# Kernel optimization log

Measured on AMD Instinct MI355X. Metric: run time of the kernel, lower is better.

## Reference

```python
import jax, jax.numpy as jnp
import numpy as np

IMG = 128                  # img_size
FMM = 35.0
SENSOR = 32.0
FUV = FMM * IMG / SENSOR   # focal length in pixels (screen space, in_ndc=False)
N_PTS = 16384
CHUNK = 1024               # points per scan step
R_SIL = 0.008              # silhouette pass radius (NDC)
R_DEP = 0.012              # depth pass radius (NDC)
K_SIL = 8
K_DEP = 16
DIST = 1.2


def _look_at(dist, elev_deg, azim_deg):
    # PyTorch3D look_at_view_transform with at=origin, up=+Y, degrees=True
    elev = jnp.deg2rad(elev_deg)
    azim = jnp.deg2rad(azim_deg)
    cam = jnp.stack([dist * jnp.cos(elev) * jnp.sin(azim),
                     dist * jnp.sin(elev),
                     dist * jnp.cos(elev) * jnp.cos(azim)], axis=-1)  # (B,3)
    up = jnp.array([0.0, 1.0, 0.0], dtype=cam.dtype)
    z_ax = -cam / (jnp.linalg.norm(cam, axis=-1, keepdims=True) + 1e-8)
    x_ax = jnp.cross(jnp.broadcast_to(up, z_ax.shape), z_ax)
    x_ax = x_ax / (jnp.linalg.norm(x_ax, axis=-1, keepdims=True) + 1e-8)
    y_ax = jnp.cross(z_ax, x_ax)
    R = jnp.stack([x_ax, y_ax, z_ax], axis=-1)   # columns are camera axes
    T = -jnp.einsum('bi,bij->bj', cam, R)        # X_cam = X_world @ R + T
    return R, T


def _project(pts, R, T):
    # world -> camera (row-vector convention) -> screen px -> PyTorch3D NDC
    Xc = jnp.einsum('bni,bij->bnj', pts, R) + T[:, None, :]
    z = Xc[..., 2]
    z_safe = jnp.where(z > 1e-5, z, 1.0)  # points behind camera are culled anyway
    xs = FUV * Xc[..., 0] / z_safe + IMG / 2.0
    ys = FUV * Xc[..., 1] / z_safe + IMG / 2.0
    x_ndc = 1.0 - 2.0 * xs / IMG
    y_ndc = 1.0 - 2.0 * ys / IMG
    return jnp.stack([x_ndc, y_ndc], axis=-1), z


def _rasterize(xy, z, r2, K):
    """Per-pixel K nearest-in-depth points within per-point NDC radius.
    xy: (B,N,2) NDC, z: (B,N) camera depth, r2: (B,N) squared radius.
    Returns zbuf, dists of shape (B,IMG,IMG,K), -1 for empty slots."""
    B, N, _ = xy.shape
    P = IMG * IMG
    # pixel-center NDC grid (PyTorch3D: +X left, +Y up; row-major flatten)
    gxs = 1.0 - (2.0 * jnp.arange(IMG, dtype=xy.dtype) + 1.0) / IMG  # per column
    gys = 1.0 - (2.0 * jnp.arange(IMG, dtype=xy.dtype) + 1.0) / IMG  # per row
    gx = jnp.tile(gxs, IMG)          # (P,)
    gy = jnp.repeat(gys, IMG)        # (P,)

    nch = N // CHUNK
    px = xy[..., 0].reshape(B, nch, CHUNK).swapaxes(0, 1)
    py = xy[..., 1].reshape(B, nch, CHUNK).swapaxes(0, 1)
    pz = z.reshape(B, nch, CHUNK).swapaxes(0, 1)
    pr2 = r2.reshape(B, nch, CHUNK).swapaxes(0, 1)

    def body(carry, c):
        top_z, top_d = carry
        cx, cy, cz, cr2 = c                               # each (B,CHUNK)
        dx = gx[None, :, None] - cx[:, None, :]           # (B,P,CHUNK)
        dy = gy[None, :, None] - cy[:, None, :]
        d2 = dx * dx + dy * dy
        ok = (d2 < cr2[:, None, :]) & (cz[:, None, :] > 0.0)
        zc = jnp.where(ok, cz[:, None, :], jnp.inf)
        cand_z = jnp.concatenate([top_z, zc], axis=-1)    # (B,P,K+CHUNK)
        cand_d = jnp.concatenate([top_d, d2], axis=-1)
        negz, idx = jax.lax.top_k(-cand_z, K)             # K smallest depths
        return (-negz, jnp.take_along_axis(cand_d, idx, axis=-1)), None

    init = (jnp.full((B, P, K), jnp.inf, dtype=xy.dtype),
            jnp.zeros((B, P, K), dtype=xy.dtype))
    (top_z, top_d), _ = jax.lax.scan(jax.checkpoint(body), init, (px, py, pz, pr2))
    valid = jnp.isfinite(top_z)
    zbuf = jnp.where(valid, top_z, -1.0).reshape(B, IMG, IMG, K)
    dists = jnp.where(valid, top_d, -1.0).reshape(B, IMG, IMG, K)
    return zbuf, dists


def setup_inputs() -> dict:
    key = jax.random.key(0)
    k1, k2 = jax.random.split(key)
    point_cloud = jax.random.normal(k1, (2, N_PTS, 6), dtype=jnp.float32) * 0.25
    param = jax.random.normal(k2, (2, 8, 3), dtype=jnp.float32) * 20.0  # degrees
    return {"point_cloud": point_cloud, "param": param}


def reference(point_cloud, param):
    pts = point_cloud[..., :3]
    B = pts.shape[0]
    elev0 = param[:, 1, 0]
    azim0 = param[:, 0, 0]

    # ---- silhouette pass (radius 0.008, K=8) + alpha compositing ----
    R0, T0 = _look_at(DIST, elev0, azim0)
    xy0, z0 = _project(pts, R0, T0)
    r2_sil = jnp.full((B, N_PTS), R_SIL * R_SIL, dtype=pts.dtype)
    _, dists_s = _rasterize(xy0, z0, r2_sil, K_SIL)
    alphas = jnp.where(dists_s >= 0.0, 1.0 - dists_s / (R_SIL * R_SIL), 0.0)
    trans = jnp.cumprod(1.0 - alphas, axis=-1)
    trans_excl = jnp.concatenate([jnp.ones_like(trans[..., :1]), trans[..., :-1]], axis=-1)
    sihlt_map = jnp.sum(alphas * trans_excl, axis=-1, keepdims=True) * 255.0  # (B,H,W,1)

    # ---- depth pass with random view (radius 0.012, K=16) ----
    kd = jax.random.key(42)
    ke, ka = jax.random.split(kd)
    elev_d = jax.random.uniform(ke, (B,), dtype=pts.dtype) * 60.0 - 30.0
    azim_d = jax.random.uniform(ka, (B,), dtype=pts.dtype) * 300.0 + azim0 + 30.0
    Rd, Td = _look_at(DIST, elev_d, azim_d)
    xyd, zd = _project(pts, Rd, Td)
    r2_dep = jnp.full((B, N_PTS), R_DEP * R_DEP, dtype=pts.dtype)
    zbuf_d, _ = _rasterize(xyd, zd, r2_dep, K_DEP)
    depth_ini = zbuf_d[..., 0]

    # density-aware adaptive radius (detached, per source .detach())
    area = jnp.sum((jax.lax.stop_gradient(depth_ini) > 0.0).astype(pts.dtype), axis=(1, 2))
    pa_radius = area / 16384.0 * 0.057                      # (B,)
    r2_ada = jnp.broadcast_to((pa_radius * pa_radius)[:, None], (B, N_PTS))

    zbuf_a, dists_a = _rasterize(xyd, zd, r2_ada, K_DEP)
    depth_img = zbuf_a[..., :8]
    dist_top = dists_a[..., :8]
    return (sihlt_map, depth_img, dist_top)
```

## Files before the change

### kernel.cpp

```cpp
#include <hip/hip_runtime.h>
#include <hip/hip_cooperative_groups.h>
#include <cstring>
#include <cstdint>

namespace cg = cooperative_groups;

#define NPTS 16384
#define FUVC 140.0f
#define R_SILF 0.008f
#define R_DEPF 0.012f
#define R2_SIL (0.008f*0.008f)
#define R2_DEP (0.012f*0.012f)
#define CH 512

#define AREA_OFF  48
#define PA_OFF    50
#define R2ADA_OFF 52
#define TICK0     54
#define TICK1     55
#define CNT_SIL   64
#define OFF_SIL   2112
#define CNT_ADA   4160
#define OFF_ADA   6208
#define FLAGS8    8256
#define FLAGS     8256
#define ZERO_END  16448
#define PROJ0     41024
#define PROJ1     172096
#define LSILF     303168
#define LADAF     827456
#define WS1_WORDS 2007104u
#define WS1_NEEDED ((size_t)WS1_WORDS * 4u)
#define LSIL      303168
#define LADA      434240
#define WS2_WORDS 729152u
#define WS2_NEEDED ((size_t)WS2_WORDS * 4u)

#define FUSED_BLOCKS 1024
#define FUSED_NT (FUSED_BLOCKS * 256)

__device__ __forceinline__ void cam_calc(float elev, float azim, float c[12]) {
    const float D2R = 0.017453292519943295f;
    float er = elev * D2R, ar = azim * D2R;
    float ce = cosf(er), se = sinf(er), ca = cosf(ar), sa = sinf(ar);
    float cx = 1.2f * ce * sa, cy = 1.2f * se, cz = 1.2f * ce * ca;
    float n = sqrtf(cx*cx + cy*cy + cz*cz) + 1e-8f;
    float zx = -cx / n, zy = -cy / n, zz = -cz / n;
    float xx = zz, xy = 0.0f, xz = -zx;
    float xn = sqrtf(xx*xx + xy*xy + xz*xz) + 1e-8f;
    xx /= xn; xz /= xn;
    float yx = zy*xz - zz*xy, yy = zz*xx - zx*xz, yz = zx*xy - zy*xx;
    c[0]=xx; c[1]=xy; c[2]=xz; c[3]=yx; c[4]=yy; c[5]=yz;
    c[6]=zx; c[7]=zy; c[8]=zz;
    c[9]  = -(cx*xx + cy*xy + cz*xz);
    c[10] = -(cx*yx + cy*yy + cz*yz);
    c[11] = -(cx*zx + cy*zy + cz*zz);
}

__device__ __forceinline__ void cam_compute(const float* __restrict__ param,
                                            float* __restrict__ ws,
                                            int t, float ue0, float ue1,
                                            float ua0, float ua1) {
    int b = t >> 1, cam = t & 1;
    float azim0 = param[b * 24 + 0];
    float elev0 = param[b * 24 + 3];
    float elev, azim;
    if (cam == 0) { elev = elev0; azim = azim0; }
    else {
        float ue = b ? ue1 : ue0;
        float ua = b ? ua1 : ua0;
        elev = ue * 60.0f - 30.0f;
        azim = ua * 300.0f + azim0 + 30.0f;
    }
    float c[12];
    cam_calc(elev, azim, c);
    float* w = ws + t * 12;
    #pragma unroll
    for (int i = 0; i < 12; i++) w[i] = c[i];
}

__device__ __forceinline__ float4 project_pt(const float* __restrict__ P,
                                             const float c[12]) {
    float X = P[0], Y = P[1], Z = P[2];
    float xc = X*c[0] + Y*c[1] + Z*c[2] + c[9];
    float yc = X*c[3] + Y*c[4] + Z*c[5] + c[10];
    float zc = X*c[6] + Y*c[7] + Z*c[8] + c[11];
    float zs = zc > 1e-5f ? zc : 1.0f;
    float px = 1.0f - (FUVC * xc / zs + 64.0f) * (1.0f/64.0f);
    float py = 1.0f - (FUVC * yc / zs + 64.0f) * (1.0f/64.0f);
    return make_float4(px, py, zc, 0.0f);
}

__device__ __forceinline__ void pix_range(float p, float r, int& lo, int& hi) {
    float lo_f = (1.0f - p - r) * 64.0f - 0.5f;
    float hi_f = (1.0f - p + r) * 64.0f - 0.5f;
    lo = (int)ceilf(lo_f - 1e-3f);
    hi = (int)floorf(hi_f + 1e-3f);
    lo = max(lo, 0); hi = min(hi, 127);
}

__device__ __forceinline__ void bin_bbox(float4 q, float r, int& bxl, int& bxh,
                                         int& byl, int& byh) {
    bxl = 0; bxh = -1; byl = 0; byh = -1;
    if (q.z > 0.0f) {
        int cl, chh, rl, rh;
        pix_range(q.x, r, cl, chh);
        pix_range(q.y, r, rl, rh);
        if (cl <= chh && rl <= rh) {
            bxl = cl >> 2; bxh = chh >> 2; byl = rl >> 2; byh = rh >> 2;
        }
    }
}

__device__ __forceinline__ void top8_insert(float z, float d,
                                            float tz[8], float td[8]) {
    #pragma unroll
    for (int k = 0; k < 8; k++) {
        bool lt = z < tz[k];
        float oz = tz[k], od = td[k];
        if (lt) { tz[k] = z; td[k] = d; z = oz; d = od; }
    }
}

__device__ __forceinline__ void hit_test(float4 pt, float gx, float gy, float r2,
                                         float tz[8], float td[8]) {
    float dx = gx - pt.x, dy = gy - pt.y;
    float d2 = dx*dx + dy*dy;
    if (d2 < r2 && pt.z > 0.0f && pt.z < tz[7]) top8_insert(pt.z, d2, tz, td);
}

__device__ __forceinline__ void merge_sorted8(float tz[8], float td[8], int mask) {
    float oz[8], od[8];
    #pragma unroll
    for (int k = 0; k < 8; k++) {
        oz[k] = __shfl_xor(tz[k], mask);
        od[k] = __shfl_xor(td[k], mask);
    }
    float mz[8], md[8];
    #pragma unroll
    for (int k = 0; k < 8; k++) {
        bool take = oz[7 - k] < tz[k];
        mz[k] = take ? oz[7 - k] : tz[k];
        md[k] = take ? od[7 - k] : td[k];
    }
    #define CE(i, j) { bool sw = mz[j] < mz[i]; \
        float t1 = mz[i], t2 = md[i]; \
        mz[i] = sw ? mz[j] : mz[i]; md[i] = sw ? md[j] : md[i]; \
        mz[j] = sw ? t1 : mz[j];    md[j] = sw ? t2 : md[j]; }
    CE(0,4) CE(1,5) CE(2,6) CE(3,7)
    CE(0,2) CE(1,3) CE(4,6) CE(5,7)
    CE(0,1) CE(2,3) CE(4,5) CE(6,7)
    #undef CE
    #pragma unroll
    for (int k = 0; k < 8; k++) { tz[k] = mz[k]; td[k] = md[k]; }
}

__device__ __forceinline__ void scan1024(unsigned* uw, unsigned cbase,
                                         unsigned obase, unsigned* s, int t) {
    unsigned c0 = uw[cbase + t*4 + 0];
    unsigned c1 = uw[cbase + t*4 + 1];
    unsigned c2 = uw[cbase + t*4 + 2];
    unsigned c3 = uw[cbase + t*4 + 3];
    unsigned tot = c0 + c1 + c2 + c3;
    s[t] = tot; __syncthreads();
    for (int off = 1; off < 256; off <<= 1) {
        unsigned v = (t >= off) ? s[t - off] : 0u;
        __syncthreads();
        s[t] += v;
        __syncthreads();
    }
    unsigned base = s[t] - tot;
    uw[obase + t*4 + 0] = base;
    uw[obase + t*4 + 1] = base + c0;
    uw[obase + t*4 + 2] = base + c0 + c1;
    uw[obase + t*4 + 3] = base + c0 + c1 + c2;
    uw[cbase + t*4 + 0] = 0;
    uw[cbase + t*4 + 1] = 0;
    uw[cbase + t*4 + 2] = 0;
    uw[cbase + t*4 + 3] = 0;
}

__device__ __forceinline__ void body_area_scan(float* __restrict__ ws, int job,
                                               int t, unsigned* s) {
    unsigned* uw = (unsigned*)ws;
    if (job < 2) {
        int b = job;
        unsigned acc = 0;
        #pragma unroll
        for (int j = 0; j < 16; j++) {
            unsigned w = uw[FLAGS8 + b * 4096 + t * 16 + j];
            acc += __popc(w & 0x01010101u);
        }
        s[t] = acc; __syncthreads();
        for (int off = 128; off > 0; off >>= 1) {
            if (t < off) s[t] += s[t + off];
            __syncthreads();
        }
        if (t == 0) {
            unsigned area = s[0];
            uw[AREA_OFF + b] = area;
            float pa = (float)area * (1.0f/16384.0f) * 0.057f;
            ws[PA_OFF + b] = pa;
            ws[R2ADA_OFF + b] = pa * pa;
        }
    } else {
        int b = job - 2;
        scan1024(uw, CNT_SIL + b * 1024, OFF_SIL + b * 1024, s, t);
    }
}

__device__ __forceinline__ void body_cnt_ada(float* __restrict__ ws, int p) {
    unsigned* uw = (unsigned*)ws;
    int b = p >> 14;
    float4 q = ((const float4*)(ws + PROJ1))[p];
    float pa = ws[PA_OFF + b];
    int bxl, bxh, byl, byh;
    bin_bbox(q, pa, bxl, bxh, byl, byh);
    for (int by = byl; by <= byh; by++)
        for (int bx = bxl; bx <= bxh; bx++)
            atomicAdd(&uw[CNT_ADA + b * 1024 + by * 32 + bx], 1u);
}

__device__ __forceinline__ void body_scat_sil(float* __restrict__ ws, int p) {
    unsigned* uw = (unsigned*)ws;
    int b = p >> 14;
    float4 q = ((const float4*)(ws + PROJ0))[p];
    int bxl, bxh, byl, byh;
    bin_bbox(q, R_SILF, bxl, bxh, byl, byh);
    for (int by = byl; by <= byh; by++)
        for (int bx = bxl; bx <= bxh; bx++) {
            unsigned bin = b * 1024 + by * 32 + bx;
            unsigned idx = uw[OFF_SIL + bin] + atomicAdd(&uw[CNT_SIL + bin], 1u);
            ((float4*)(ws + LSILF))[b * 65536 + idx] = q;
        }
}

__device__ __forceinline__ void body_scan_ada(float* __restrict__ ws, int b, int t) {
    unsigned* uw = (unsigned*)ws;
    unsigned c[16]; unsigned tot = 0;
    #pragma unroll
    for (int j = 0; j < 16; j++) { c[j] = uw[CNT_ADA + b * 1024 + t * 16 + j]; tot += c[j]; }
    unsigned inc = tot;
    #pragma unroll
    for (int off = 1; off < 64; off <<= 1) {
        unsigned v = __shfl_up(inc, off);
        if (t >= off) inc += v;
    }
    unsigned base = inc - tot;
    #pragma unroll
    for (int j = 0; j < 16; j++) {
        uw[OFF_ADA + b * 1024 + t * 16 + j] = base;
        base += c[j];
        uw[CNT_ADA + b * 1024 + t * 16 + j] = 0u;
    }
}

__device__ __forceinline__ void body_scat_ada(float* __restrict__ ws, int p) {
    unsigned* uw = (unsigned*)ws;
    int b = p >> 14;
    float4 q = ((const float4*)(ws + PROJ1))[p];
    float pa = ws[PA_OFF + b];
    int bxl, bxh, byl, byh;
    bin_bbox(q, pa, bxl, bxh, byl, byh);
    for (int by = byl; by <= byh; by++)
        for (int bx = bxl; bx <= bxh; bx++) {
            unsigned bin = b * 1024 + by * 32 + bx;
            unsigned idx = uw[OFF_ADA + bin] + atomicAdd(&uw[CNT_ADA + bin], 1u);
            ((float4*)(ws + LADAF))[b * 147456 + idx] = q;
        }
}

__device__ __forceinline__ void body_gather(const float* __restrict__ ws,
                                            float* __restrict__ out,
                                            int id, int lane) {
    const unsigned* uw = (const unsigned*)ws;
    bool sil = id < 2048;
    int gt = sil ? id : id - 2048;
    int b = gt >> 10;
    int tile = gt & 1023;
    int p = lane & 15, s = lane >> 4;
    int bx = tile & 31, by = tile >> 5;
    int col = (bx << 2) + (p & 3), row = (by << 2) + (p >> 2);
    float gx = 1.0f - (float)(2*col + 1) * (1.0f/128.0f);
    float gy = 1.0f - (float)(2*row + 1) * (1.0f/128.0f);
    float r2 = sil ? R2_SIL : ws[R2ADA_OFF + b];
    unsigned start = sil ? uw[OFF_SIL + b * 1024 + tile] : uw[OFF_ADA + b * 1024 + tile];
    unsigned len   = sil ? uw[CNT_SIL + b * 1024 + tile] : uw[CNT_ADA + b * 1024 + tile];
    const float4* lst = sil ? ((const float4*)(ws + LSILF)) + b * 65536 + start
                            : ((const float4*)(ws + LADAF)) + b * 147456 + start;

    float tz[8], td[8];
    #pragma unroll
    for (int k = 0; k < 8; k++) { tz[k] = INFINITY; td[k] = 0.0f; }

    unsigned i = (unsigned)s;
    while (i + 28 < len) {
        float4 cb[8];
        #pragma unroll
        for (int u = 0; u < 8; u++) cb[u] = lst[i + 4u * (unsigned)u];
        #pragma unroll
        for (int u = 0; u < 8; u++) hit_test(cb[u], gx, gy, r2, tz, td);
        i += 32;
    }
    for (; i < len; i += 4) hit_test(lst[i], gx, gy, r2, tz, td);

    merge_sorted8(tz, td, 16);
    merge_sorted8(tz, td, 32);

    if (s == 0) {
        int pix = (b << 14) + row * 128 + col;
        if (sil) {
            float trans = 1.0f, acc = 0.0f;
            #pragma unroll
            for (int k = 0; k < 8; k++) {
                float a = (tz[k] != INFINITY) ? (1.0f - td[k] / R2_SIL) : 0.0f;
                acc += a * trans;
                trans *= (1.0f - a);
            }
            out[pix] = acc * 255.0f;
        } else {
            float* dep = out + 32768  + (size_t)pix * 8;
            float* dst = out + 294912 + (size_t)pix * 8;
            #pragma unroll
            for (int k = 0; k < 8; k++) {
                bool v = (tz[k] != INFINITY);
                dep[k] = v ? tz[k] : -1.0f;
                dst[k] = v ? td[k] : -1.0f;
            }
        }
    }
}

__global__ __launch_bounds__(256) void k_fusedp(const float* __restrict__ pc,
                                                const float* __restrict__ param,
                                                float* __restrict__ ws,
                                                float* __restrict__ out,
                                                float ue0, float ue1,
                                                float ua0, float ua1) {
    cg::grid_group grid = cg::this_grid();
    unsigned* uw = (unsigned*)ws;
    __shared__ unsigned sh[2048];
    __shared__ unsigned shLast;
    int t = threadIdx.x;
    int tid = blockIdx.x * 256 + t;

    for (int i = 48 + tid; i < ZERO_END; i += FUSED_NT) uw[i] = 0u;
    if (tid < 4) cam_compute(param, ws, tid, ue0, ue1, ua0, ua1);
    grid.sync();

    if (blockIdx.x < 128) {
        int b = blockIdx.x >> 6;
        int p = ((blockIdx.x & 63) << 8) + t;
        unsigned char* fb = (unsigned char*)(uw + FLAGS8);
        const float* P = pc + ((size_t)b * NPTS + p) * 6;
        float c0[12], c1[12];
        const float* w0 = ws + (b * 2) * 12;
        #pragma unroll
        for (int i = 0; i < 12; i++) { c0[i] = w0[i]; c1[i] = w0[12 + i]; }

        #pragma unroll
        for (int j = 0; j < 4; j++) sh[t * 4 + j] = 0u;
        __syncthreads();

        float4 q0 = project_pt(P, c0);
        ((float4*)(ws + PROJ0))[b * NPTS + p] = q0;
        int bxl, bxh, byl, byh;
        bin_bbox(q0, R_SILF, bxl, bxh, byl, byh);
        for (int by = byl; by <= byh; by++)
            for (int bx = bxl; bx <= bxh; bx++)
                atomicAdd(&sh[by * 32 + bx], 1u);

        float4 q1 = project_pt(P, c1);
        ((float4*)(ws + PROJ1))[b * NPTS + p] = q1;
        if (q1.z > 0.0f) {
            int cl, chh, rl, rh;
            pix_range(q1.x, R_DEPF, cl, chh);
            pix_range(q1.y, R_DEPF, rl, rh);
            for (int rr = rl; rr <= rh; rr++) {
                float gyv = 1.0f - (float)(2 * rr + 1) * (1.0f/128.0f);
                float dy = gyv - q1.y;
                for (int cc = cl; cc <= chh; cc++) {
                    float gxv = 1.0f - (float)(2 * cc + 1) * (1.0f/128.0f);
                    float dx = gxv - q1.x;
                    if (dx*dx + dy*dy < R2_DEP) fb[b * NPTS + rr * 128 + cc] = 1;
                }
            }
        }
        __syncthreads();
        #pragma unroll
        for (int j = 0; j < 4; j++) {
            unsigned c = sh[t * 4 + j];
            if (c) atomicAdd(&uw[CNT_SIL + b * 1024 + t * 4 + j], c);
        }
        __threadfence();
    }
    if (t == 0) shLast = (atomicAdd(&uw[TICK0], 1u) == FUSED_BLOCKS - 1) ? 1u : 0u;
    __syncthreads();
    if (shLast) {
        __threadfence();
        for (int job = 0; job < 4; job++) {
            body_area_scan(ws, job, t, sh);
            __syncthreads();
        }
        __threadfence();
    }
    grid.sync();

    if (blockIdx.x < 128) {
        int b = blockIdx.x >> 6;
        int p = ((blockIdx.x & 63) << 8) + t;
        float4 q = ((const float4*)(ws + PROJ1))[b * NPTS + p];
        float pa = ws[PA_OFF + b];
        #pragma unroll
        for (int j = 0; j < 4; j++) sh[t * 4 + j] = 0u;
        __syncthreads();
        int bxl, bxh, byl, byh;
        bin_bbox(q, pa, bxl, bxh, byl, byh);
        for (int by = byl; by <= byh; by++)
            for (int bx = bxl; bx <= bxh; bx++)
                atomicAdd(&sh[by * 32 + bx], 1u);
        __syncthreads();
        #pragma unroll
        for (int j = 0; j < 4; j++) {
            unsigned c = sh[t * 4 + j];
            if (c) atomicAdd(&uw[CNT_ADA + b * 1024 + t * 4 + j], c);
        }
        __threadfence();
    } else if (blockIdx.x < 256) {
        int blk = blockIdx.x - 128;
        int b = blk >> 6;
        int p = ((blk & 63) << 8) + t;
        float4 q = ((const float4*)(ws + PROJ0))[b * NPTS + p];
        int bxl, bxh, byl, byh;
        bin_bbox(q, R_SILF, bxl, bxh, byl, byh);
        #pragma unroll
        for (int j = 0; j < 4; j++) sh[t * 4 + j] = 0u;
        __syncthreads();
        for (int by = byl; by <= byh; by++)
            for (int bx = bxl; bx <= bxh; bx++)
                atomicAdd(&sh[by * 32 + bx], 1u);
        __syncthreads();
        #pragma unroll
        for (int j = 0; j < 4; j++) {
            int bin = t * 4 + j;
            unsigned c = sh[bin];
            unsigned gb = 0;
            if (c) gb = uw[OFF_SIL + b * 1024 + bin] +
                        atomicAdd(&uw[CNT_SIL + b * 1024 + bin], c);
            sh[1024 + bin] = gb;
            sh[bin] = 0u;
        }
        __syncthreads();
        for (int by = byl; by <= byh; by++)
            for (int bx = bxl; bx <= bxh; bx++) {
                int bin = by * 32 + bx;
                unsigned loc = atomicAdd(&sh[bin], 1u);
                ((float4*)(ws + LSILF))[b * 65536 + sh[1024 + bin] + loc] = q;
            }
        __threadfence();
    }
    if (t == 0) shLast = (atomicAdd(&uw[TICK1], 1u) == FUSED_BLOCKS - 1) ? 1u : 0u;
    __syncthreads();
    if (shLast) {
        __threadfence();
        if (t < 128) body_scan_ada(ws, t >> 6, t & 63);
        __threadfence();
    }
    grid.sync();

    if (blockIdx.x < 128) {
        int b = blockIdx.x >> 6;
        int p = ((blockIdx.x & 63) << 8) + t;
        float4 q = ((const float4*)(ws + PROJ1))[b * NPTS + p];
        float pa = ws[PA_OFF + b];
        int bxl, bxh, byl, byh;
        bin_bbox(q, pa, bxl, bxh, byl, byh);
        #pragma unroll
        for (int j = 0; j < 4; j++) sh[t * 4 + j] = 0u;
        __syncthreads();
        for (int by = byl; by <= byh; by++)
            for (int bx = bxl; bx <= bxh; bx++)
                atomicAdd(&sh[by * 32 + bx], 1u);
        __syncthreads();
        #pragma unroll
        for (int j = 0; j < 4; j++) {
            int bin = t * 4 + j;
            unsigned c = sh[bin];
            unsigned gb = 0;
            if (c) gb = uw[OFF_ADA + b * 1024 + bin] +
                        atomicAdd(&uw[CNT_ADA + b * 1024 + bin], c);
            sh[1024 + bin] = gb;
            sh[bin] = 0u;
        }
        __syncthreads();
        for (int by = byl; by <= byh; by++)
            for (int bx = bxl; bx <= bxh; bx++) {
                int bin = by * 32 + bx;
                unsigned loc = atomicAdd(&sh[bin], 1u);
                ((float4*)(ws + LADAF))[b * 147456 + sh[1024 + bin] + loc] = q;
            }
    }
    grid.sync();

    body_gather(ws, out, tid >> 6, tid & 63);
}


__global__ __launch_bounds__(256) void k_zero(float* __restrict__ ws) {
    unsigned* uw = (unsigned*)ws;
    int gid = blockIdx.x * 256 + threadIdx.x;
    int stride = gridDim.x * 256;
    for (int i = 48 + gid; i < ZERO_END; i += stride) uw[i] = 0u;
}

__global__ __launch_bounds__(256) void k_proj_v3(const float* __restrict__ pc,
                                                 const float* __restrict__ param,
                                                 float* __restrict__ ws,
                                                 float ue0, float ue1,
                                                 float ua0, float ua1) {
    int b = blockIdx.x >> 6;
    int p = ((blockIdx.x & 63) << 8) + threadIdx.x;
    float azim0 = param[b * 24 + 0];
    float elev0 = param[b * 24 + 3];
    float c0[12], c1[12];
    cam_calc(elev0, azim0, c0);
    float ue = b ? ue1 : ue0;
    float ua = b ? ua1 : ua0;
    cam_calc(ue * 60.0f - 30.0f, ua * 300.0f + azim0 + 30.0f, c1);

    unsigned* uw = (unsigned*)ws;
    unsigned char* fb = (unsigned char*)(uw + FLAGS8);
    const float* P = pc + ((size_t)b * NPTS + p) * 6;

    float4 q0 = project_pt(P, c0);
    ((float4*)(ws + PROJ0))[b * NPTS + p] = q0;
    int bxl, bxh, byl, byh;
    bin_bbox(q0, R_SILF, bxl, bxh, byl, byh);
    for (int by = byl; by <= byh; by++)
        for (int bx = bxl; bx <= bxh; bx++)
            atomicAdd(&uw[CNT_SIL + b * 1024 + by * 32 + bx], 1u);

    float4 q1 = project_pt(P, c1);
    ((float4*)(ws + PROJ1))[b * NPTS + p] = q1;
    if (q1.z > 0.0f) {
        int cl, chh, rl, rh;
        pix_range(q1.x, R_DEPF, cl, chh);
        pix_range(q1.y, R_DEPF, rl, rh);
        for (int rr = rl; rr <= rh; rr++) {
            float gy = 1.0f - (float)(2 * rr + 1) * (1.0f/128.0f);
            float dy = gy - q1.y;
            for (int cc = cl; cc <= chh; cc++) {
                float gx = 1.0f - (float)(2 * cc + 1) * (1.0f/128.0f);
                float dx = gx - q1.x;
                if (dx*dx + dy*dy < R2_DEP) fb[b * NPTS + rr * 128 + cc] = 1;
            }
        }
    }
}

__global__ __launch_bounds__(256) void k_area_scan_v3(float* __restrict__ ws) {
    __shared__ unsigned s[256];
    body_area_scan(ws, blockIdx.x, threadIdx.x, s);
}

__global__ __launch_bounds__(64) void k_cntada_scatsil(float* __restrict__ ws) {
    int id = blockIdx.x;
    bool isCnt = id < 512;
    int p = ((isCnt ? id : id - 512) << 6) + threadIdx.x;
    if (isCnt) body_cnt_ada(ws, p);
    else       body_scat_sil(ws, p);
}

__global__ __launch_bounds__(64) void k_scan_ada64(float* __restrict__ ws) {
    body_scan_ada(ws, blockIdx.x, threadIdx.x);
}

__global__ __launch_bounds__(64) void k_scatter_ada_v2(float* __restrict__ ws) {
    body_scat_ada(ws, (blockIdx.x << 6) + threadIdx.x);
}

__global__ __launch_bounds__(64) void k_gather_v3(const float* __restrict__ ws,
                                                  float* __restrict__ out) {
    body_gather(ws, out, blockIdx.x, threadIdx.x);
}


__global__ __launch_bounds__(256) void k_init(const float* __restrict__ param,
                                              float* __restrict__ ws,
                                              float ue0, float ue1,
                                              float ua0, float ua1) {
    unsigned* uw = (unsigned*)ws;
    int gid = blockIdx.x * 256 + threadIdx.x;
    int stride = gridDim.x * 256;
    for (int i = gid; i < 2048; i += stride) { uw[CNT_SIL + i] = 0u; uw[CNT_ADA + i] = 0u; }
    for (int i = gid; i < 32768; i += stride) uw[FLAGS + i] = 0u;
    if (gid < 2) uw[AREA_OFF + gid] = 0u;
    if (gid < 4) cam_compute(param, ws, gid, ue0, ue1, ua0, ua1);
}

__global__ __launch_bounds__(256) void k_proj_count(const float* __restrict__ pc,
                                                    float* __restrict__ ws) {
    unsigned* uw = (unsigned*)ws;
    int b = blockIdx.x >> 6;
    int p = ((blockIdx.x & 63) << 8) + threadIdx.x;
    const float* P = pc + ((size_t)b * NPTS + p) * 6;
    float c0[12], c1[12];
    const float* w0 = ws + (b * 2) * 12;
    #pragma unroll
    for (int i = 0; i < 12; i++) { c0[i] = w0[i]; c1[i] = w0[12 + i]; }

    float4 q0 = project_pt(P, c0);
    ((float4*)(ws + PROJ0))[b * NPTS + p] = q0;
    int bxl, bxh, byl, byh;
    bin_bbox(q0, R_SILF, bxl, bxh, byl, byh);
    for (int by = byl; by <= byh; by++)
        for (int bx = bxl; bx <= bxh; bx++)
            atomicAdd(&uw[CNT_SIL + b * 1024 + by * 32 + bx], 1u);

    float4 q1 = project_pt(P, c1);
    ((float4*)(ws + PROJ1))[b * NPTS + p] = q1;
    if (q1.z > 0.0f) {
        int cl, chh, rl, rh;
        pix_range(q1.x, R_DEPF, cl, chh);
        pix_range(q1.y, R_DEPF, rl, rh);
        for (int rr = rl; rr <= rh; rr++) {
            float gy = 1.0f - (float)(2 * rr + 1) * (1.0f/128.0f);
            float dy = gy - q1.y;
            for (int cc = cl; cc <= chh; cc++) {
                float gx = 1.0f - (float)(2 * cc + 1) * (1.0f/128.0f);
                float dx = gx - q1.x;
                if (dx*dx + dy*dy < R2_DEP) uw[FLAGS + b * NPTS + rr * 128 + cc] = 1u;
            }
        }
    }
}

__global__ __launch_bounds__(256) void k_area_scan(float* __restrict__ ws) {
    unsigned* uw = (unsigned*)ws;
    __shared__ unsigned s[256];
    int t = threadIdx.x;
    int job = blockIdx.x;
    if (job < 2) {
        int b = job;
        unsigned acc = 0;
        for (int i = t; i < NPTS; i += 256) acc += uw[FLAGS + b * NPTS + i];
        s[t] = acc; __syncthreads();
        for (int off = 128; off > 0; off >>= 1) {
            if (t < off) s[t] += s[t + off];
            __syncthreads();
        }
        if (t == 0) {
            unsigned area = s[0];
            uw[AREA_OFF + b] = area;
            float pa = (float)area * (1.0f/16384.0f) * 0.057f;
            ws[PA_OFF + b] = pa;
            ws[R2ADA_OFF + b] = pa * pa;
        }
    } else {
        int b = job - 2;
        scan1024(uw, CNT_SIL + b * 1024, OFF_SIL + b * 1024, s, t);
    }
}

__global__ __launch_bounds__(256) void k_count_ada(float* __restrict__ ws) {
    int b = blockIdx.x >> 6;
    int p = ((blockIdx.x & 63) << 8) + threadIdx.x;
    body_cnt_ada(ws, b * NPTS + p);
}

__global__ __launch_bounds__(256) void k_scan_ada(float* __restrict__ ws) {
    unsigned* uw = (unsigned*)ws;
    __shared__ unsigned s[256];
    int b = blockIdx.x;
    scan1024(uw, CNT_ADA + b * 1024, OFF_ADA + b * 1024, s, threadIdx.x);
}

__global__ __launch_bounds__(256) void k_scatter(float* __restrict__ ws) {
    unsigned* uw = (unsigned*)ws;
    int b = blockIdx.x >> 6;
    int p = ((blockIdx.x & 63) << 8) + threadIdx.x;

    float4 q0 = ((const float4*)(ws + PROJ0))[b * NPTS + p];
    int bxl, bxh, byl, byh;
    bin_bbox(q0, R_SILF, bxl, bxh, byl, byh);
    for (int by = byl; by <= byh; by++)
        for (int bx = bxl; bx <= bxh; bx++) {
            unsigned bin = b * 1024 + by * 32 + bx;
            unsigned idx = uw[OFF_SIL + bin] + atomicAdd(&uw[CNT_SIL + bin], 1u);
            uw[LSIL + b * 65536 + idx] = (unsigned)p;
        }

    float4 q1 = ((const float4*)(ws + PROJ1))[b * NPTS + p];
    float pa = ws[PA_OFF + b];
    bin_bbox(q1, pa, bxl, bxh, byl, byh);
    for (int by = byl; by <= byh; by++)
        for (int bx = bxl; bx <= bxh; bx++) {
            unsigned bin = b * 1024 + by * 32 + bx;
            unsigned idx = uw[OFF_ADA + bin] + atomicAdd(&uw[CNT_ADA + bin], 1u);
            uw[LADA + b * 147456 + idx] = (unsigned)p;
        }
}

__global__ __launch_bounds__(256) void k_gather_sil(const float* __restrict__ ws,
                                                    float* __restrict__ out) {
    const unsigned* uw = (const unsigned*)ws;
    int b = blockIdx.x >> 6;
    int tile = (blockIdx.x & 63) * 16 + (threadIdx.x >> 4);
    int q = threadIdx.x & 15;
    int bx = tile & 31, by = tile >> 5;
    int col = (bx << 2) + (q & 3), row = (by << 2) + (q >> 2);
    float gx = 1.0f - (float)(2*col + 1) * (1.0f/128.0f);
    float gy = 1.0f - (float)(2*row + 1) * (1.0f/128.0f);
    unsigned start = uw[OFF_SIL + b * 1024 + tile];
    unsigned len   = uw[CNT_SIL + b * 1024 + tile];
    const float4* pr = (const float4*)(ws + PROJ0) + b * NPTS;

    float tz[8], td[8];
    #pragma unroll
    for (int k = 0; k < 8; k++) { tz[k] = INFINITY; td[k] = 0.0f; }
    for (unsigned i = 0; i < len; i++) {
        unsigned pid = uw[LSIL + b * 65536 + start + i];
        hit_test(pr[pid], gx, gy, R2_SIL, tz, td);
    }
    float trans = 1.0f, s = 0.0f;
    #pragma unroll
    for (int k = 0; k < 8; k++) {
        float a = (tz[k] != INFINITY) ? (1.0f - td[k] / R2_SIL) : 0.0f;
        s += a * trans;
        trans *= (1.0f - a);
    }
    out[(b << 14) + row * 128 + col] = s * 255.0f;
}

__global__ __launch_bounds__(256) void k_gather_ada(const float* __restrict__ ws,
                                                    float* __restrict__ out) {
    const unsigned* uw = (const unsigned*)ws;
    int b = blockIdx.x >> 6;
    int tile = (blockIdx.x & 63) * 16 + (threadIdx.x >> 4);
    int q = threadIdx.x & 15;
    int bx = tile & 31, by = tile >> 5;
    int col = (bx << 2) + (q & 3), row = (by << 2) + (q >> 2);
    float gx = 1.0f - (float)(2*col + 1) * (1.0f/128.0f);
    float gy = 1.0f - (float)(2*row + 1) * (1.0f/128.0f);
    float r2 = ws[R2ADA_OFF + b];
    unsigned start = uw[OFF_ADA + b * 1024 + tile];
    unsigned len   = uw[CNT_ADA + b * 1024 + tile];
    const float4* pr = (const float4*)(ws + PROJ1) + b * NPTS;

    float tz[8], td[8];
    #pragma unroll
    for (int k = 0; k < 8; k++) { tz[k] = INFINITY; td[k] = 0.0f; }
    for (unsigned i = 0; i < len; i++) {
        unsigned pid = uw[LADA + b * 147456 + start + i];
        hit_test(pr[pid], gx, gy, r2, tz, td);
    }
    int pix = (b << 14) + row * 128 + col;
    float* dep = out + 32768  + (size_t)pix * 8;
    float* dst = out + 294912 + (size_t)pix * 8;
    #pragma unroll
    for (int k = 0; k < 8; k++) {
        bool v = (tz[k] != INFINITY);
        dep[k] = v ? tz[k] : -1.0f;
        dst[k] = v ? td[k] : -1.0f;
    }
}

__global__ void cam_kernel_fb(const float* __restrict__ param, float* __restrict__ ws,
                              float ue0, float ue1, float ua0, float ua1) {
    int t = threadIdx.x;
    if (t < 2) ws[48 + t] = 0.0f;
    if (t >= 4) return;
    cam_compute(param, ws, t, ue0, ue1, ua0, ua1);
}

__device__ __forceinline__ void stage_points(const float* __restrict__ pcb,
                                             const float c[12], int c0, float4* sp) {
    for (int i = threadIdx.x; i < CH; i += 256) {
        const float* P = pcb + (size_t)(c0 + i) * 6;
        sp[i] = project_pt(P, c);
    }
}

__global__ __launch_bounds__(256) void raster_AB(const float* __restrict__ pc,
                                                 float* __restrict__ ws,
                                                 float* __restrict__ out) {
    __shared__ float4 sp[CH];
    int bid = blockIdx.x;
    bool silMode = bid < 128;
    int q = silMode ? bid : bid - 128;
    int b = q >> 6;
    int p = ((q & 63) << 8) + threadIdx.x;
    const float* cw = ws + (b * 2 + (silMode ? 0 : 1)) * 12;
    float c[12];
    #pragma unroll
    for (int i = 0; i < 12; i++) c[i] = cw[i];
    float r2 = silMode ? R2_SIL : R2_DEP;
    int col = p & 127, row = p >> 7;
    float gx = 1.0f - (float)(2*col + 1) * (1.0f/128.0f);
    float gy = 1.0f - (float)(2*row + 1) * (1.0f/128.0f);
    const float* pcb = pc + (size_t)b * NPTS * 6;

    if (silMode) {
        float tz[8], td[8];
        #pragma unroll
        for (int k = 0; k < 8; k++) { tz[k] = INFINITY; td[k] = 0.0f; }
        for (int c0 = 0; c0 < NPTS; c0 += CH) {
            __syncthreads();
            stage_points(pcb, c, c0, sp);
            __syncthreads();
            #pragma unroll 4
            for (int j = 0; j < CH; j++) hit_test(sp[j], gx, gy, r2, tz, td);
        }
        float trans = 1.0f, s = 0.0f;
        #pragma unroll
        for (int k = 0; k < 8; k++) {
            float a = (tz[k] != INFINITY) ? (1.0f - td[k] / r2) : 0.0f;
            s += a * trans;
            trans *= (1.0f - a);
        }
        out[(b << 14) + p] = s * 255.0f;
    } else {
        float mz = INFINITY;
        for (int c0 = 0; c0 < NPTS; c0 += CH) {
            __syncthreads();
            stage_points(pcb, c, c0, sp);
            __syncthreads();
            #pragma unroll 4
            for (int j = 0; j < CH; j++) {
                float4 pt = sp[j];
                float dx = gx - pt.x, dy = gy - pt.y;
                float d2 = dx*dx + dy*dy;
                if (d2 < r2 && pt.z > 0.0f) mz = fminf(mz, pt.z);
            }
        }
        unsigned long long m = __ballot(mz != INFINITY);
        if ((threadIdx.x & 63) == 0)
            atomicAdd(ws + 48 + b, (float)__popcll(m));
    }
}

__global__ __launch_bounds__(256) void raster_C(const float* __restrict__ pc,
                                                const float* __restrict__ ws,
                                                float* __restrict__ out) {
    __shared__ float4 sp[CH];
    int bid = blockIdx.x;
    int b = bid >> 6;
    int p = ((bid & 63) << 8) + threadIdx.x;
    const float* cw = ws + (b * 2 + 1) * 12;
    float c[12];
    #pragma unroll
    for (int i = 0; i < 12; i++) c[i] = cw[i];
    float area = ws[48 + b];
    float pa = (area * (1.0f/16384.0f)) * 0.057f;
    float r2 = pa * pa;
    int col = p & 127, row = p >> 7;
    float gx = 1.0f - (float)(2*col + 1) * (1.0f/128.0f);
    float gy = 1.0f - (float)(2*row + 1) * (1.0f/128.0f);
    const float* pcb = pc + (size_t)b * NPTS * 6;

    float tz[8], td[8];
    #pragma unroll
    for (int k = 0; k < 8; k++) { tz[k] = INFINITY; td[k] = 0.0f; }
    for (int c0 = 0; c0 < NPTS; c0 += CH) {
        __syncthreads();
        stage_points(pcb, c, c0, sp);
        __syncthreads();
        #pragma unroll 4
        for (int j = 0; j < CH; j++) hit_test(sp[j], gx, gy, r2, tz, td);
    }
    float* dep = out + 32768  + (size_t)((b << 14) + p) * 8;
    float* dst = out + 294912 + (size_t)((b << 14) + p) * 8;
    #pragma unroll
    for (int k = 0; k < 8; k++) {
        bool v = (tz[k] != INFINITY);
        dep[k] = v ? tz[k] : -1.0f;
        dst[k] = v ? td[k] : -1.0f;
    }
}

static inline uint32_t rotl32(uint32_t x, int r) { return (x << r) | (x >> (32 - r)); }

static void tf2x32(uint32_t k0, uint32_t k1, uint32_t c0, uint32_t c1,
                   uint32_t* o0, uint32_t* o1) {
    uint32_t ks0 = k0, ks1 = k1, ks2 = k0 ^ k1 ^ 0x1BD11BDAu;
    uint32_t x0 = c0 + ks0, x1 = c1 + ks1;
    static const int rA[4] = {13, 15, 26, 6};
    static const int rB[4] = {17, 29, 16, 24};
    #define RND4(R) do { for (int i = 0; i < 4; i++) { x0 += x1; x1 = rotl32(x1, R[i]); x1 ^= x0; } } while (0)
    RND4(rA); x0 += ks1; x1 += ks2 + 1u;
    RND4(rB); x0 += ks2; x1 += ks0 + 2u;
    RND4(rA); x0 += ks0; x1 += ks1 + 3u;
    RND4(rB); x0 += ks1; x1 += ks2 + 4u;
    RND4(rA); x0 += ks2; x1 += ks0 + 5u;
    #undef RND4
    *o0 = x0; *o1 = x1;
}

static inline float bits_to_unit_float(uint32_t bits) {
    uint32_t fb = (bits >> 9) | 0x3f800000u;
    float f;
    memcpy(&f, &fb, 4);
    return f - 1.0f;
}

extern "C" void kernel_launch(void* const* d_in, const int* in_sizes, int n_in,
                              void* d_out, int out_size, void* d_ws, size_t ws_size,
                              hipStream_t stream) {
    const float* pc    = (const float*)d_in[0];
    const float* param = (const float*)d_in[1];
    float* out = (float*)d_out;
    float* ws  = (float*)d_ws;

    uint32_t ke0, ke1, ka0, ka1, b1, b2;
    tf2x32(0u, 42u, 0u, 0u, &ke0, &ke1);
    tf2x32(0u, 42u, 0u, 1u, &ka0, &ka1);
    float ue[2], ua[2];
    for (uint32_t i = 0; i < 2; i++) {
        tf2x32(ke0, ke1, 0u, i, &b1, &b2);
        ue[i] = bits_to_unit_float(b1 ^ b2);
        tf2x32(ka0, ka1, 0u, i, &b1, &b2);
        ua[i] = bits_to_unit_float(b1 ^ b2);
    }
    float ue0 = ue[0], ue1 = ue[1], ua0 = ua[0], ua1 = ua[1];

    if (ws_size >= WS1_NEEDED) {
        int dev = 0;
        hipGetDevice(&dev);
        hipDeviceProp_t prop;
        bool coop = (hipGetDeviceProperties(&prop, dev) == hipSuccess) &&
                    prop.cooperativeLaunch;
        if (coop) {
            int maxB = 0;
            if (hipOccupancyMaxActiveBlocksPerMultiprocessor(&maxB, k_fusedp, 256, 0)
                    != hipSuccess ||
                maxB * prop.multiProcessorCount < FUSED_BLOCKS)
                coop = false;
        }
        if (coop) {
            void* args[] = { (void*)&pc, (void*)&param, (void*)&ws, (void*)&out,
                             (void*)&ue0, (void*)&ue1, (void*)&ua0, (void*)&ua1 };
            hipError_t e = hipLaunchCooperativeKernel((const void*)k_fusedp,
                                                      dim3(FUSED_BLOCKS), dim3(256),
                                                      args, 0, stream);
            if (e == hipSuccess) return;
        }
        k_zero          <<<16, 256, 0, stream>>>(ws);
        k_proj_v3       <<<128, 256, 0, stream>>>(pc, param, ws, ue0, ue1, ua0, ua1);
        k_area_scan_v3  <<<4, 256, 0, stream>>>(ws);
        k_cntada_scatsil<<<1024, 64, 0, stream>>>(ws);
        k_scan_ada64    <<<2, 64, 0, stream>>>(ws);
        k_scatter_ada_v2<<<512, 64, 0, stream>>>(ws);
        k_gather_v3     <<<4096, 64, 0, stream>>>(ws, out);
    } else if (ws_size >= WS2_NEEDED) {
        k_init      <<<64, 256, 0, stream>>>(param, ws, ue0, ue1, ua0, ua1);
        k_proj_count<<<128, 256, 0, stream>>>(pc, ws);
        k_area_scan <<<4, 256, 0, stream>>>(ws);
        k_count_ada <<<128, 256, 0, stream>>>(ws);
        k_scan_ada  <<<2, 256, 0, stream>>>(ws);
        k_scatter   <<<128, 256, 0, stream>>>(ws);
        k_gather_sil<<<128, 256, 0, stream>>>(ws, out);
        k_gather_ada<<<128, 256, 0, stream>>>(ws, out);
    } else {
        cam_kernel_fb<<<1, 64, 0, stream>>>(param, ws, ue0, ue1, ua0, ua1);
        raster_AB<<<256, 256, 0, stream>>>(pc, ws, out);
        raster_C <<<128, 256, 0, stream>>>(pc, ws, out);
    }
}
```

Before: 92.52 us.

## Split each tile's gather across four wavefronts with shared-memory top-8 merge

The gather stage now gives each 4x4 pixel tile a 256-thread block instead of one 64-lane wavefront, so 16 segments per pixel scan the bin list. Each wavefront merges its partial top-8 lists with shuffles, then lane-0 threads merge the four wavefront results through shared memory. In the cooperative fused kernel each block loops over four tiles to cover them all. The aim is more parallelism and memory-level overlap on long bin lists, in exchange for extra merge work, block barriers and shared-memory traffic.

```diff
diff --git a/kernel.cpp b/kernel.cpp
--- a/kernel.cpp
+++ b/kernel.cpp
@@ -129,6 +129,11 @@
     if (d2 < r2 && pt.z > 0.0f && pt.z < tz[7]) top8_insert(pt.z, d2, tz, td);
 }
 
+#define CE8(i, j) { bool sw = mz[j] < mz[i]; \
+    float t1 = mz[i], t2 = md[i]; \
+    mz[i] = sw ? mz[j] : mz[i]; md[i] = sw ? md[j] : md[i]; \
+    mz[j] = sw ? t1 : mz[j];    md[j] = sw ? t2 : md[j]; }
+
 __device__ __forceinline__ void merge_sorted8(float tz[8], float td[8], int mask) {
     float oz[8], od[8];
     #pragma unroll
@@ -143,14 +148,27 @@
         mz[k] = take ? oz[7 - k] : tz[k];
         md[k] = take ? od[7 - k] : td[k];
     }
-    #define CE(i, j) { bool sw = mz[j] < mz[i]; \
-        float t1 = mz[i], t2 = md[i]; \
-        mz[i] = sw ? mz[j] : mz[i]; md[i] = sw ? md[j] : md[i]; \
-        mz[j] = sw ? t1 : mz[j];    md[j] = sw ? t2 : md[j]; }
-    CE(0,4) CE(1,5) CE(2,6) CE(3,7)
-    CE(0,2) CE(1,3) CE(4,6) CE(5,7)
-    CE(0,1) CE(2,3) CE(4,5) CE(6,7)
-    #undef CE
+    CE8(0,4) CE8(1,5) CE8(2,6) CE8(3,7)
+    CE8(0,2) CE8(1,3) CE8(4,6) CE8(5,7)
+    CE8(0,1) CE8(2,3) CE8(4,5) CE8(6,7)
+    #pragma unroll
+    for (int k = 0; k < 8; k++) { tz[k] = mz[k]; td[k] = md[k]; }
+}
+
+__device__ __forceinline__ void merge_seq8(float tz[8], float td[8],
+                                           const float* __restrict__ ozp,
+                                           const float* __restrict__ odp) {
+    float mz[8], md[8];
+    #pragma unroll
+    for (int k = 0; k < 8; k++) {
+        float oz = ozp[7 - k], od = odp[7 - k];
+        bool take = oz < tz[k];
+        mz[k] = take ? oz : tz[k];
+        md[k] = take ? od : td[k];
+    }
+    CE8(0,4) CE8(1,5) CE8(2,6) CE8(3,7)
+    CE8(0,2) CE8(1,3) CE8(4,6) CE8(5,7)
+    CE8(0,1) CE8(2,3) CE8(4,5) CE8(6,7)
     #pragma unroll
     for (int k = 0; k < 8; k++) { tz[k] = mz[k]; td[k] = md[k]; }
 }
@@ -268,6 +286,80 @@
             unsigned idx = uw[OFF_ADA + bin] + atomicAdd(&uw[CNT_ADA + bin], 1u);
             ((float4*)(ws + LADAF))[b * 147456 + idx] = q;
         }
+}
+
+__device__ __forceinline__ void body_gather256(const float* __restrict__ ws,
+                                               float* __restrict__ out,
+                                               int id, int t,
+                                               float* __restrict__ sm) {
+    const unsigned* uw = (const unsigned*)ws;
+    bool sil = id < 2048;
+    int gt = sil ? id : id - 2048;
+    int b = gt >> 10;
+    int tile = gt & 1023;
+    int p = t & 15, seg = t >> 4;
+    int bx = tile & 31, by = tile >> 5;
+    int col = (bx << 2) + (p & 3), row = (by << 2) + (p >> 2);
+    float gx = 1.0f - (float)(2*col + 1) * (1.0f/128.0f);
+    float gy = 1.0f - (float)(2*row + 1) * (1.0f/128.0f);
+    float r2 = sil ? R2_SIL : ws[R2ADA_OFF + b];
+    unsigned start = sil ? uw[OFF_SIL + b * 1024 + tile] : uw[OFF_ADA + b * 1024 + tile];
+    unsigned len   = sil ? uw[CNT_SIL + b * 1024 + tile] : uw[CNT_ADA + b * 1024 + tile];
+    const float4* lst = sil ? ((const float4*)(ws + LSILF)) + b * 65536 + start
+                            : ((const float4*)(ws + LADAF)) + b * 147456 + start;
+
+    float tz[8], td[8];
+    #pragma unroll
+    for (int k = 0; k < 8; k++) { tz[k] = INFINITY; td[k] = 0.0f; }
+
+    unsigned i = (unsigned)seg;
+    while (i + 112 < len) {
+        float4 cb[8];
+        #pragma unroll
+        for (int u = 0; u < 8; u++) cb[u] = lst[i + 16u * (unsigned)u];
+        #pragma unroll
+        for (int u = 0; u < 8; u++) hit_test(cb[u], gx, gy, r2, tz, td);
+        i += 128;
+    }
+    for (; i < len; i += 16) hit_test(lst[i], gx, gy, r2, tz, td);
+
+    merge_sorted8(tz, td, 16);
+    merge_sorted8(tz, td, 32);
+
+    int w = t >> 6;
+    if ((t & 63) < 16) {
+        float* dst = sm + (w * 16 + p) * 16;
+        #pragma unroll
+        for (int k = 0; k < 8; k++) { dst[k] = tz[k]; dst[8 + k] = td[k]; }
+    }
+    __syncthreads();
+    if (t < 16) {
+        #pragma unroll
+        for (int ww = 1; ww < 4; ww++) {
+            const float* src = sm + (ww * 16 + p) * 16;
+            merge_seq8(tz, td, src, src + 8);
+        }
+        int pix = (b << 14) + row * 128 + col;
+        if (sil) {
+            float trans = 1.0f, acc = 0.0f;
+            #pragma unroll
+            for (int k = 0; k < 8; k++) {
+                float a = (tz[k] != INFINITY) ? (1.0f - td[k] / R2_SIL) : 0.0f;
+                acc += a * trans;
+                trans *= (1.0f - a);
+            }
+            out[pix] = acc * 255.0f;
+        } else {
+            float* dep = out + 32768  + (size_t)pix * 8;
+            float* dst = out + 294912 + (size_t)pix * 8;
+            #pragma unroll
+            for (int k = 0; k < 8; k++) {
+                bool v = (tz[k] != INFINITY);
+                dep[k] = v ? tz[k] : -1.0f;
+                dst[k] = v ? td[k] : -1.0f;
+            }
+        }
+    }
 }
 
 __device__ __forceinline__ void body_gather(const float* __restrict__ ws,
@@ -502,7 +594,11 @@
     }
     grid.sync();
 
-    body_gather(ws, out, tid >> 6, tid & 63);
+    for (int rep = 0; rep < 4; rep++) {
+        int id = rep * 1024 + blockIdx.x;
+        body_gather256(ws, out, id, t, (float*)sh);
+        __syncthreads();
+    }
 }
 
 
@@ -579,9 +675,10 @@
     body_scat_ada(ws, (blockIdx.x << 6) + threadIdx.x);
 }
 
-__global__ __launch_bounds__(64) void k_gather_v3(const float* __restrict__ ws,
-                                                  float* __restrict__ out) {
-    body_gather(ws, out, blockIdx.x, threadIdx.x);
+__global__ __launch_bounds__(256) void k_gather_v4(const float* __restrict__ ws,
+                                                   float* __restrict__ out) {
+    __shared__ float sm[1024];
+    body_gather256(ws, out, blockIdx.x, threadIdx.x, sm);
 }
 
 
@@ -950,7 +1047,7 @@
         k_cntada_scatsil<<<1024, 64, 0, stream>>>(ws);
         k_scan_ada64    <<<2, 64, 0, stream>>>(ws);
         k_scatter_ada_v2<<<512, 64, 0, stream>>>(ws);
-        k_gather_v3     <<<4096, 64, 0, stream>>>(ws, out);
+        k_gather_v4     <<<4096, 256, 0, stream>>>(ws, out);
     } else if (ws_size >= WS2_NEEDED) {
         k_init      <<<64, 256, 0, stream>>>(param, ws, ue0, ue1, ua0, ua1);
         k_proj_count<<<128, 256, 0, stream>>>(pc, ws);
```

Result: faster. 85.72 us (-7.4%).
